# Kernel tuning notes

Measured on AMD Instinct MI355X. Metric: run time of the kernel, lower is better.

## Reference

```python
import jax, jax.numpy as jnp
import numpy as np

N = 262144          # flattened node batch
IN_S, IN_V = 256, 32
OUT_S, OUT_V = 256, 32
H = max(IN_V, OUT_V)  # 32
EPS = 1e-4


def setup_inputs() -> dict:
    key = jax.random.key(0)
    ks = jax.random.split(key, 8)
    inv = lambda f: 1.0 / np.sqrt(f).astype(np.float32)
    return {
        "s": jax.random.normal(ks[0], (N, IN_S), jnp.float32),
        "V": jax.random.normal(ks[1], (N, IN_V, 3), jnp.float32),
        "W_h": jax.random.normal(ks[2], (H, IN_V), jnp.float32) * inv(IN_V),
        "W_mu": jax.random.normal(ks[3], (OUT_V, H), jnp.float32) * inv(H),
        "W_m_w": jax.random.normal(ks[4], (OUT_S, H + IN_S), jnp.float32) * inv(H + IN_S),
        "W_m_b": jax.random.normal(ks[5], (OUT_S,), jnp.float32) * 0.01,
        "W_g_w": jax.random.normal(ks[6], (OUT_V, OUT_S), jnp.float32) * inv(OUT_S),
        "W_g_b": jax.random.normal(ks[7], (OUT_V,), jnp.float32) * 0.01,
    }


def reference(s, V, W_h, W_mu, W_m_w, W_m_b, W_g_w, W_g_b):
    # V_h = W_h @ V : [N, H, 3]
    V_h = jnp.einsum('hv,nvc->nhc', W_h, V)
    # per-row L2 norm, clipped at eps : [N, H]
    s_h = jnp.maximum(jnp.linalg.norm(V_h, axis=-1), EPS)
    # Linear on concatenated scalars : [N, OUT_S]
    s_m = jnp.concatenate([s, s_h], axis=-1) @ W_m_w.T + W_m_b
    s_dash = jax.nn.relu(s_m)                      # sigma = relu
    # V_mu = W_mu @ V_h : [N, OUT_V, 3]
    V_mu = jnp.einsum('mh,nhc->nmc', W_mu, V_h)
    # vector gate: sigmoid(W_g(sigmoid(s_m)))  (sigma_plus = sigmoid)
    gate = jax.nn.sigmoid(jax.nn.sigmoid(s_m) @ W_g_w.T + W_g_b)  # [N, OUT_V]
    V_dash = gate[..., None] * V_mu
    return s_dash, V_dash
```

## Files before the change

### kernel.cpp

```cpp
#include <hip/hip_runtime.h>

#define NTOT 262144
#define BN   32
#define NT   256
#define SXS  296
#define VTS  36

typedef __attribute__((ext_vector_type(8))) short bf16x8;
typedef __attribute__((ext_vector_type(4))) float f32x4;

static __device__ __forceinline__ unsigned short f2b(float x) {
    union { float f; unsigned u; } c; c.f = x;
    unsigned r = c.u + 0x7FFFu + ((c.u >> 16) & 1u);
    return (unsigned short)(r >> 16);
}
static __device__ __forceinline__ float b2f(unsigned short h) {
    union { unsigned u; float f; } c; c.u = ((unsigned)h) << 16; return c.f;
}
static __device__ __forceinline__ bf16x8 cvt8(const float* p) {
    float4 x = *(const float4*)p, y = *(const float4*)(p + 4);
    bf16x8 r;
    r[0] = (short)f2b(x.x); r[1] = (short)f2b(x.y); r[2] = (short)f2b(x.z); r[3] = (short)f2b(x.w);
    r[4] = (short)f2b(y.x); r[5] = (short)f2b(y.y); r[6] = (short)f2b(y.z); r[7] = (short)f2b(y.w);
    return r;
}
static __device__ __forceinline__ void glds16(const unsigned short* g, void* l) {
    __builtin_amdgcn_global_load_lds(
        (const __attribute__((address_space(1))) void*)g,
        (__attribute__((address_space(3))) void*)l, 16, 0, 0);
}

__global__ void pack_w(const float* __restrict__ Wmw, const float* __restrict__ Wgw,
                       unsigned short* __restrict__ wp) {
    int t = blockIdx.x * 256 + threadIdx.x;
    if (t < 73728) {
        int o = t / 288, k = t % 288;
        int ks = k >> 5, kk = k & 31, ch = o >> 7, ol = o & 127;
        int kks = kk ^ (((ol >> 1) & 3) << 3);
        wp[(ks * 2 + ch) * 4096 + ol * 32 + kks] = f2b(Wmw[t]);
    } else if (t < 81920) {
        int j = t - 73728;
        int o = j >> 8, k = j & 255;
        wp[73728 + (k >> 5) * 1024 + o * 32 + (k & 31)] = f2b(Wgw[j]);
    }
}

template<int USE_WS>
__global__ __launch_bounds__(NT, 3)
void gvp_main(const float* __restrict__ s, const float* __restrict__ V,
              const float* __restrict__ Wh, const float* __restrict__ Wmu,
              const float* __restrict__ Wmw, const float* __restrict__ Wmb,
              const float* __restrict__ Wgw, const float* __restrict__ Wgb,
              const unsigned short* __restrict__ wpack,
              float* __restrict__ out)
{
    __shared__ __attribute__((aligned(16))) unsigned short sX[BN * SXS];
    __shared__ __attribute__((aligned(16))) unsigned short sWb[2 * 4096];
    __shared__ __attribute__((aligned(16))) unsigned short sVT[96 * VTS];

    const int t  = threadIdx.x;
    const int w  = t >> 6, l = t & 63;
    const int fr = l & 15, fq = l >> 4;
    const int n0 = blockIdx.x * BN;
    const int half = w & 1, oh = w >> 1;

    if (USE_WS) {
        const unsigned short* src = wpack + w * 1024 + l * 8;
        unsigned short* dst = sWb + w * 1024;
        glds16(src, dst);
        glds16(src + 512, dst + 512);
    }

    #pragma unroll
    for (int i = 0; i < 8; ++i) {
        int n = i * 4 + w;
        float4 x4 = *(const float4*)&s[(size_t)(n0 + n) * 256 + 4 * l];
        ushort4 h4; h4.x = f2b(x4.x); h4.y = f2b(x4.y); h4.z = f2b(x4.z); h4.w = f2b(x4.w);
        *(ushort4*)&sX[n * SXS + 4 * l] = h4;
    }
    {
        int n = t >> 3, vq = t & 7;
        const float* p = &V[(size_t)(n0 + n) * 96 + vq * 12];
        float4 q0 = *(const float4*)(p);
        float4 q1 = *(const float4*)(p + 4);
        float4 q2 = *(const float4*)(p + 8);
        ushort4 c0 = { f2b(q0.x), f2b(q0.w), f2b(q1.z), f2b(q2.y) };
        ushort4 c1 = { f2b(q0.y), f2b(q1.x), f2b(q1.w), f2b(q2.z) };
        ushort4 c2 = { f2b(q0.z), f2b(q1.y), f2b(q2.x), f2b(q2.w) };
        *(ushort4*)&sVT[(0 * 32 + n) * VTS + vq * 4] = c0;
        *(ushort4*)&sVT[(1 * 32 + n) * VTS + vq * 4] = c1;
        *(ushort4*)&sVT[(2 * 32 + n) * VTS + vq * 4] = c2;
    }
    if (!USE_WS) {
        int ol = w * 32 + (l >> 1), kh = l & 1, x = (ol >> 1) & 3;
        const float* p = &Wmw[ol * 288 + kh * 16];
        *(bf16x8*)&sWb[ol * 32 + (((kh * 2 + 0) ^ x) << 3)] = cvt8(p);
        *(bf16x8*)&sWb[ol * 32 + (((kh * 2 + 1) ^ x) << 3)] = cvt8(p + 8);
    }
    __syncthreads();

    {
        bf16x8 bh = cvt8(&Wh[(oh * 16 + fr) * 32 + fq * 8]);
        f32x4 va0 = {0,0,0,0}, va1 = {0,0,0,0}, va2 = {0,0,0,0};
        bf16x8 a0 = *(const bf16x8*)&sVT[(0 * 32 + half * 16 + fr) * VTS + fq * 8];
        bf16x8 a1 = *(const bf16x8*)&sVT[(1 * 32 + half * 16 + fr) * VTS + fq * 8];
        bf16x8 a2 = *(const bf16x8*)&sVT[(2 * 32 + half * 16 + fr) * VTS + fq * 8];
        va0 = __builtin_amdgcn_mfma_f32_16x16x32_bf16(a0, bh, va0, 0, 0, 0);
        va1 = __builtin_amdgcn_mfma_f32_16x16x32_bf16(a1, bh, va1, 0, 0, 0);
        va2 = __builtin_amdgcn_mfma_f32_16x16x32_bf16(a2, bh, va2, 0, 0, 0);
        __syncthreads();
        #pragma unroll
        for (int r = 0; r < 4; ++r) {
            int nl = half * 16 + fq * 4 + r;
            int h  = oh * 16 + fr;
            sVT[(0 * 32 + nl) * VTS + h] = f2b(va0[r]);
            sVT[(1 * 32 + nl) * VTS + h] = f2b(va1[r]);
            sVT[(2 * 32 + nl) * VTS + h] = f2b(va2[r]);
            float nrm = sqrtf(fmaf(va0[r], va0[r], fmaf(va1[r], va1[r], va2[r] * va2[r])));
            sX[nl * SXS + 256 + h] = f2b(fmaxf(nrm, 1e-4f));
        }
    }
    __syncthreads();

    f32x4 acc[2][4];
    #pragma unroll
    for (int mt = 0; mt < 2; ++mt)
        #pragma unroll
        for (int j = 0; j < 4; ++j) acc[mt][j] = (f32x4){0.f, 0.f, 0.f, 0.f};

    const int ol0 = w * 32 + fr, ol1 = ol0 + 16;
    const int bo0 = ol0 * 32 + ((fq ^ ((ol0 >> 1) & 3)) << 3);
    const int bo1 = ol1 * 32 + ((fq ^ ((ol1 >> 1) & 3)) << 3);

    #pragma unroll
    for (int it = 0; it < 18; ++it) {
        if (it < 17) {
            if (USE_WS) {
                const unsigned short* src = wpack + (it + 1) * 4096 + w * 1024 + l * 8;
                unsigned short* dst = sWb + ((it + 1) & 1) * 4096 + w * 1024;
                glds16(src, dst);
                glds16(src + 512, dst + 512);
            } else {
                int it1 = it + 1, ks1 = it1 >> 1, ch1 = it1 & 1;
                int ol = w * 32 + (l >> 1), kh = l & 1, x = (ol >> 1) & 3;
                const float* p = &Wmw[(ch1 * 128 + ol) * 288 + ks1 * 32 + kh * 16];
                unsigned short* dst = sWb + (it1 & 1) * 4096;
                *(bf16x8*)&dst[ol * 32 + (((kh * 2 + 0) ^ x) << 3)] = cvt8(p);
                *(bf16x8*)&dst[ol * 32 + (((kh * 2 + 1) ^ x) << 3)] = cvt8(p + 8);
            }
        }
        const int ks = it >> 1;
        const unsigned short* bw = sWb + (it & 1) * 4096;
        bf16x8 a0 = *(const bf16x8*)&sX[fr * SXS + ks * 32 + fq * 8];
        bf16x8 a1 = *(const bf16x8*)&sX[(16 + fr) * SXS + ks * 32 + fq * 8];
        bf16x8 b0 = *(const bf16x8*)&bw[bo0];
        bf16x8 b1 = *(const bf16x8*)&bw[bo1];
        const int ji = (it & 1) * 2;
        acc[0][ji + 0] = __builtin_amdgcn_mfma_f32_16x16x32_bf16(a0, b0, acc[0][ji + 0], 0, 0, 0);
        acc[1][ji + 0] = __builtin_amdgcn_mfma_f32_16x16x32_bf16(a1, b0, acc[1][ji + 0], 0, 0, 0);
        acc[0][ji + 1] = __builtin_amdgcn_mfma_f32_16x16x32_bf16(a0, b1, acc[0][ji + 1], 0, 0, 0);
        acc[1][ji + 1] = __builtin_amdgcn_mfma_f32_16x16x32_bf16(a1, b1, acc[1][ji + 1], 0, 0, 0);
        __syncthreads();
    }

    float bias[4];
    #pragma unroll
    for (int ji = 0; ji < 4; ++ji)
        bias[ji] = Wmb[(ji >> 1) * 128 + w * 32 + (ji & 1) * 16 + fr];

    float* sRel = (float*)sWb;
    #pragma unroll
    for (int mt = 0; mt < 2; ++mt) {
        #pragma unroll
        for (int r = 0; r < 4; ++r) {
            int row  = fq * 4 + r;
            int node = mt * 16 + row;
            #pragma unroll
            for (int ji = 0; ji < 4; ++ji) {
                int col = (ji >> 1) * 128 + w * 32 + (ji & 1) * 16 + fr;
                float m = acc[mt][ji][r] + bias[ji];
                sX[node * SXS + col] = f2b(1.f / (1.f + __expf(-m)));
                sRel[row * 256 + col] = fmaxf(m, 0.f);
            }
        }
        __syncthreads();
        #pragma unroll
        for (int i = 0; i < 4; ++i) {
            int flat = i * NT + t;
            int row = flat >> 6, c4 = flat & 63;
            float4 v4 = *(const float4*)&sRel[row * 256 + c4 * 4];
            *(float4*)&out[(size_t)(n0 + mt * 16 + row) * 256 + c4 * 4] = v4;
        }
        __syncthreads();
    }

    {
        const int gmt = w & 1, gnt = w >> 1;
        f32x4 g = (f32x4){0.f, 0.f, 0.f, 0.f};
        #pragma unroll
        for (int ks = 0; ks < 8; ++ks) {
            bf16x8 a = *(const bf16x8*)&sX[(gmt * 16 + fr) * SXS + ks * 32 + fq * 8];
            bf16x8 b;
            if (USE_WS) b = *(const bf16x8*)&wpack[73728 + ks * 1024 + (gnt * 16 + fr) * 32 + fq * 8];
            else        b = cvt8(&Wgw[(gnt * 16 + fr) * 256 + ks * 32 + fq * 8]);
            g = __builtin_amdgcn_mfma_f32_16x16x32_bf16(a, b, g, 0, 0, 0);
        }
        int mo = gnt * 16 + fr;
        float gb = Wgb[mo];
        #pragma unroll
        for (int r = 0; r < 4; ++r) {
            int node = gmt * 16 + fq * 4 + r;
            sX[node * SXS + 256 + mo] = f2b(1.f / (1.f + __expf(-(g[r] + gb))));
        }
    }
    __syncthreads();

    float* sc = (float*)sWb;
    {
        bf16x8 bm = cvt8(&Wmu[(oh * 16 + fr) * 32 + fq * 8]);
        f32x4 m0 = {0,0,0,0}, m1 = {0,0,0,0}, m2 = {0,0,0,0};
        bf16x8 a0 = *(const bf16x8*)&sVT[(0 * 32 + half * 16 + fr) * VTS + fq * 8];
        bf16x8 a1 = *(const bf16x8*)&sVT[(1 * 32 + half * 16 + fr) * VTS + fq * 8];
        bf16x8 a2 = *(const bf16x8*)&sVT[(2 * 32 + half * 16 + fr) * VTS + fq * 8];
        m0 = __builtin_amdgcn_mfma_f32_16x16x32_bf16(a0, bm, m0, 0, 0, 0);
        m1 = __builtin_amdgcn_mfma_f32_16x16x32_bf16(a1, bm, m1, 0, 0, 0);
        m2 = __builtin_amdgcn_mfma_f32_16x16x32_bf16(a2, bm, m2, 0, 0, 0);
        #pragma unroll
        for (int r = 0; r < 4; ++r) {
            int node = half * 16 + fq * 4 + r;
            int m    = oh * 16 + fr;
            float g  = b2f(sX[node * SXS + 256 + m]);
            sc[node * 96 + m * 3 + 0] = g * m0[r];
            sc[node * 96 + m * 3 + 1] = g * m1[r];
            sc[node * 96 + m * 3 + 2] = g * m2[r];
        }
    }
    __syncthreads();
    const size_t VBASE = (size_t)NTOT * 256;
    #pragma unroll
    for (int i = 0; i < 3; ++i) {
        int f = i * NT + t;
        *(float4*)&out[VBASE + (size_t)n0 * 96 + f * 4] = *(const float4*)&sc[f * 4];
    }
}

extern "C" void kernel_launch(void* const* d_in, const int* in_sizes, int n_in,
                              void* d_out, int out_size, void* d_ws, size_t ws_size,
                              hipStream_t stream) {
    const float* s   = (const float*)d_in[0];
    const float* V   = (const float*)d_in[1];
    const float* Wh  = (const float*)d_in[2];
    const float* Wmu = (const float*)d_in[3];
    const float* Wmw = (const float*)d_in[4];
    const float* Wmb = (const float*)d_in[5];
    const float* Wgw = (const float*)d_in[6];
    const float* Wgb = (const float*)d_in[7];
    float* out = (float*)d_out;

    dim3 grid(NTOT / BN);
    dim3 block(NT);

    if (ws_size >= 163840) {
        pack_w<<<320, 256, 0, stream>>>(Wmw, Wgw, (unsigned short*)d_ws);
        gvp_main<1><<<grid, block, 0, stream>>>(s, V, Wh, Wmu, Wmw, Wmb, Wgw, Wgb,
                                                (const unsigned short*)d_ws, out);
    } else {
        gvp_main<0><<<grid, block, 0, stream>>>(s, V, Wh, Wmu, Wmw, Wmb, Wgw, Wgb,
                                                nullptr, out);
    }
}
```

Baseline: 219.6 us.

## Deepen weight prefetch to two stages, drop per-iteration barriers, swizzle relu staging

```diff
diff --git a/kernel.cpp b/kernel.cpp
--- a/kernel.cpp
+++ b/kernel.cpp
@@ -65,10 +65,13 @@
     const int half = w & 1, oh = w >> 1;
 
     if (USE_WS) {
-        const unsigned short* src = wpack + w * 1024 + l * 8;
-        unsigned short* dst = sWb + w * 1024;
-        glds16(src, dst);
-        glds16(src + 512, dst + 512);
+        #pragma unroll
+        for (int c = 0; c < 2; ++c) {
+            const unsigned short* src = wpack + c * 4096 + w * 1024 + l * 8;
+            unsigned short* dst = sWb + c * 4096 + w * 1024;
+            glds16(src, dst);
+            glds16(src + 512, dst + 512);
+        }
     }
 
     #pragma unroll
@@ -92,10 +95,14 @@
         *(ushort4*)&sVT[(2 * 32 + n) * VTS + vq * 4] = c2;
     }
     if (!USE_WS) {
-        int ol = w * 32 + (l >> 1), kh = l & 1, x = (ol >> 1) & 3;
-        const float* p = &Wmw[ol * 288 + kh * 16];
-        *(bf16x8*)&sWb[ol * 32 + (((kh * 2 + 0) ^ x) << 3)] = cvt8(p);
-        *(bf16x8*)&sWb[ol * 32 + (((kh * 2 + 1) ^ x) << 3)] = cvt8(p + 8);
+        #pragma unroll
+        for (int c = 0; c < 2; ++c) {
+            int ol = w * 32 + (l >> 1), kh = l & 1, x = (ol >> 1) & 3;
+            const float* p = &Wmw[(c * 128 + ol) * 288 + kh * 16];
+            unsigned short* dst = sWb + c * 4096;
+            *(bf16x8*)&dst[ol * 32 + (((kh * 2 + 0) ^ x) << 3)] = cvt8(p);
+            *(bf16x8*)&dst[ol * 32 + (((kh * 2 + 1) ^ x) << 3)] = cvt8(p + 8);
+        }
     }
     __syncthreads();
 
@@ -134,20 +141,10 @@
 
     #pragma unroll
     for (int it = 0; it < 18; ++it) {
-        if (it < 17) {
-            if (USE_WS) {
-                const unsigned short* src = wpack + (it + 1) * 4096 + w * 1024 + l * 8;
-                unsigned short* dst = sWb + ((it + 1) & 1) * 4096 + w * 1024;
-                glds16(src, dst);
-                glds16(src + 512, dst + 512);
-            } else {
-                int it1 = it + 1, ks1 = it1 >> 1, ch1 = it1 & 1;
-                int ol = w * 32 + (l >> 1), kh = l & 1, x = (ol >> 1) & 3;
-                const float* p = &Wmw[(ch1 * 128 + ol) * 288 + ks1 * 32 + kh * 16];
-                unsigned short* dst = sWb + (it1 & 1) * 4096;
-                *(bf16x8*)&dst[ol * 32 + (((kh * 2 + 0) ^ x) << 3)] = cvt8(p);
-                *(bf16x8*)&dst[ol * 32 + (((kh * 2 + 1) ^ x) << 3)] = cvt8(p + 8);
-            }
+        if (it >= 2) {
+            if (it <= 16) asm volatile("s_waitcnt vmcnt(2)" ::: "memory");
+            else          asm volatile("s_waitcnt vmcnt(0)" ::: "memory");
+            __builtin_amdgcn_sched_barrier(0);
         }
         const int ks = it >> 1;
         const unsigned short* bw = sWb + (it & 1) * 4096;
@@ -155,19 +152,37 @@
         bf16x8 a1 = *(const bf16x8*)&sX[(16 + fr) * SXS + ks * 32 + fq * 8];
         bf16x8 b0 = *(const bf16x8*)&bw[bo0];
         bf16x8 b1 = *(const bf16x8*)&bw[bo1];
+        if (it < 16) {
+            asm volatile("s_waitcnt lgkmcnt(0)" ::: "memory");
+            __builtin_amdgcn_sched_barrier(0);
+            if (USE_WS) {
+                const unsigned short* src = wpack + (it + 2) * 4096 + w * 1024 + l * 8;
+                unsigned short* dst = sWb + (it & 1) * 4096 + w * 1024;
+                glds16(src, dst);
+                glds16(src + 512, dst + 512);
+            } else {
+                int it2 = it + 2, ks2 = it2 >> 1, ch2 = it2 & 1;
+                int ol = w * 32 + (l >> 1), kh = l & 1, x = (ol >> 1) & 3;
+                const float* p = &Wmw[(ch2 * 128 + ol) * 288 + ks2 * 32 + kh * 16];
+                unsigned short* dst = sWb + (it & 1) * 4096;
+                *(bf16x8*)&dst[ol * 32 + (((kh * 2 + 0) ^ x) << 3)] = cvt8(p);
+                *(bf16x8*)&dst[ol * 32 + (((kh * 2 + 1) ^ x) << 3)] = cvt8(p + 8);
+            }
+        }
         const int ji = (it & 1) * 2;
         acc[0][ji + 0] = __builtin_amdgcn_mfma_f32_16x16x32_bf16(a0, b0, acc[0][ji + 0], 0, 0, 0);
         acc[1][ji + 0] = __builtin_amdgcn_mfma_f32_16x16x32_bf16(a1, b0, acc[1][ji + 0], 0, 0, 0);
         acc[0][ji + 1] = __builtin_amdgcn_mfma_f32_16x16x32_bf16(a0, b1, acc[0][ji + 1], 0, 0, 0);
         acc[1][ji + 1] = __builtin_amdgcn_mfma_f32_16x16x32_bf16(a1, b1, acc[1][ji + 1], 0, 0, 0);
-        __syncthreads();
-    }
+    }
+    __syncthreads();
 
     float bias[4];
     #pragma unroll
     for (int ji = 0; ji < 4; ++ji)
         bias[ji] = Wmb[(ji >> 1) * 128 + w * 32 + (ji & 1) * 16 + fr];
 
+    const int skw = ((fq & 1) << 4) | ((fq >> 1) << 3);
     float* sRel = (float*)sWb;
     #pragma unroll
     for (int mt = 0; mt < 2; ++mt) {
@@ -180,7 +195,7 @@
                 int col = (ji >> 1) * 128 + w * 32 + (ji & 1) * 16 + fr;
                 float m = acc[mt][ji][r] + bias[ji];
                 sX[node * SXS + col] = f2b(1.f / (1.f + __expf(-m)));
-                sRel[row * 256 + col] = fmaxf(m, 0.f);
+                sRel[row * 256 + (col ^ skw)] = fmaxf(m, 0.f);
             }
         }
         __syncthreads();
@@ -188,7 +203,8 @@
         for (int i = 0; i < 4; ++i) {
             int flat = i * NT + t;
             int row = flat >> 6, c4 = flat & 63;
-            float4 v4 = *(const float4*)&sRel[row * 256 + c4 * 4];
+            int sk2 = (((row >> 2) & 1) << 4) | (((row >> 3) & 1) << 3);
+            float4 v4 = *(const float4*)&sRel[row * 256 + ((c4 * 4) ^ sk2)];
             *(float4*)&out[(size_t)(n0 + mt * 16 + row) * 256 + c4 * 4] = v4;
         }
         __syncthreads();
```

Result: faster. 208.7 us, median of 2 (-4.9%).
